# Optimization experiments

Hardware: AMD Instinct MI355X
Metric: run time of the kernel (lower is better)

Reference implementation:

```python
import jax, jax.numpy as jnp
import numpy as np

N_FEATURES = 1024
N_HEADS = 16
D_ATTN = 64


def setup_inputs() -> dict:
    key = jax.random.key(0)
    k_x, k_qkv, k_pw, k_pb = jax.random.split(key, 4)
    B, S = 2, 2048
    x = jax.random.normal(k_x, (B, S, N_FEATURES), dtype=jnp.float32)
    # torch nn.Linear weights are [out, in]; init scale ~ 1/sqrt(in)
    w_qkv = jax.random.normal(k_qkv, (3 * N_HEADS * D_ATTN, N_FEATURES), dtype=jnp.float32) / np.sqrt(N_FEATURES)
    w_proj = jax.random.normal(k_pw, (N_FEATURES, N_HEADS * D_ATTN), dtype=jnp.float32) / np.sqrt(N_HEADS * D_ATTN)
    b_proj = jax.random.normal(k_pb, (N_FEATURES,), dtype=jnp.float32) / np.sqrt(N_HEADS * D_ATTN)
    return {"x": x, "w_qkv": w_qkv, "w_proj": w_proj, "b_proj": b_proj}


def reference(x, w_qkv, w_proj, b_proj):
    B, S, F = x.shape
    H, D = N_HEADS, D_ATTN
    # fused QKV projection (bias=False): [B,S,3*H*D]
    qkv = jnp.einsum('bsf,of->bso', x, w_qkv)
    qkv = qkv.reshape(B, S, 3, H, D)
    q = jnp.transpose(qkv[:, :, 0], (0, 2, 1, 3))  # [B,H,S,D]
    k = jnp.transpose(qkv[:, :, 1], (0, 2, 1, 3))
    v = jnp.transpose(qkv[:, :, 2], (0, 2, 1, 3))
    scale = 1.0 / jnp.sqrt(jnp.asarray(D, dtype=x.dtype))
    scores = jnp.einsum('bhqd,bhkd->bhqk', q, k) * scale  # [B,H,S,S]
    attn = jax.nn.softmax(scores, axis=-1)
    out = jnp.einsum('bhqk,bhkd->bhqd', attn, v)  # [B,H,S,D]
    out = jnp.transpose(out, (0, 2, 1, 3)).reshape(B, S, H * D)
    # output projection (dropout is identity in eval mode)
    return jnp.einsum('bsm,fm->bsf', out, w_proj) + b_proj
```

## Files before the change

kernel.cpp:

```cpp
#include <hip/hip_runtime.h>
#include <hip/hip_bf16.h>
#include <math.h>

#define BATCH 2
#define SEQ 2048
#define NFEAT 1024
#define NHEAD 16
#define DHEAD 64
#define MROWS (BATCH * SEQ)
#define NQKV (3 * NHEAD * DHEAD)

typedef __attribute__((ext_vector_type(8))) short short8;
typedef __attribute__((ext_vector_type(4))) float floatx4;

#define CEXP 0.18033688f

__device__ __forceinline__ unsigned short f2bf(float f) {
    unsigned int u = __float_as_uint(f);
    u += 0x7fff + ((u >> 16) & 1);
    return (unsigned short)(u >> 16);
}

__device__ __forceinline__ float fast_exp2(float x) {
    return __builtin_amdgcn_exp2f(x);
}

__device__ __forceinline__ uint pack_bf16x2(float lo, float hi) {
    float2 t; t.x = lo; t.y = hi;
    __hip_bfloat162 h = __float22bfloat162_rn(t);
    union { __hip_bfloat162 h; uint u; } c; c.h = h;
    return c.u;
}

__device__ __forceinline__ void async16(const void* g, void* l) {
    __builtin_amdgcn_global_load_lds(
        (const __attribute__((address_space(1))) void*)g,
        (__attribute__((address_space(3))) void*)l, 16, 0, 0);
}

__global__ void cvt_swz(const float* __restrict__ x, const float* __restrict__ wq,
                        const float* __restrict__ wp,
                        ushort* __restrict__ xb, ushort* __restrict__ wqb,
                        ushort* __restrict__ wpb) {
    const int NX = MROWS * NFEAT / 4, NWQ = NQKV * NFEAT / 4, NWP = NFEAT * NFEAT / 4;
    int i = blockIdx.x * blockDim.x + threadIdx.x;
    if (i >= NX + NWQ + NWP) return;
    const float* src; ushort* dst; int idx4;
    if (i < NX)            { src = x;  dst = xb;  idx4 = i; }
    else if (i < NX + NWQ) { src = wq; dst = wqb; idx4 = i - NX; }
    else                   { src = wp; dst = wpb; idx4 = i - NX - NWQ; }
    float4 v = ((const float4*)src)[idx4];
    ushort4 o;
    o.x = f2bf(v.x); o.y = f2bf(v.y); o.z = f2bf(v.z); o.w = f2bf(v.w);
    const int e = idx4 * 4;
    const int k = e & (NFEAT - 1);
    const int row = e >> 10;
    const int kp = (k & ~31) | (((((k >> 3) & 3) ^ ((row >> 1) & 3))) << 3) | (k & 7);
    *(ushort4*)(dst + (size_t)row * NFEAT + kp) = o;
}

__global__ __launch_bounds__(256, 2)
void gemm_qkv(const ushort* __restrict__ A, const ushort* __restrict__ W,
              ushort* __restrict__ qb, ushort* __restrict__ kb, ushort* __restrict__ vtb) {
    __shared__ ushort smem[8192];
    ushort* As = smem;
    ushort* Bs = smem + 4096;
    const int tid = threadIdx.x;
    const int wave = tid >> 6, lane = tid & 63;
    const int m0 = blockIdx.y * 128, n0 = blockIdx.x * 128;
    const int wm = (wave >> 1) * 64, wn = (wave & 1) * 64;
    const int lr = lane & 15, lg = lane >> 4;
    const int kswz = (lg ^ ((lr >> 1) & 3)) * 8;

    floatx4 acc[4][4] = {};

    const int seg0 = tid, seg1 = tid + 256;
    const int row0 = seg0 >> 2, cb0 = (seg0 & 3) * 8;
    const int row1 = seg1 >> 2, cb1 = (seg1 & 3) * 8;

    for (int k0 = 0; k0 < NFEAT; k0 += 32) {
        async16(A + (size_t)(m0 + row0) * NFEAT + k0 + cb0, (void*)(As + seg0 * 8));
        async16(A + (size_t)(m0 + row1) * NFEAT + k0 + cb1, (void*)(As + seg1 * 8));
        async16(W + (size_t)(n0 + row0) * NFEAT + k0 + cb0, (void*)(Bs + seg0 * 8));
        async16(W + (size_t)(n0 + row1) * NFEAT + k0 + cb1, (void*)(Bs + seg1 * 8));
        __syncthreads();
        short8 a[4], b[4];
#pragma unroll
        for (int i = 0; i < 4; ++i)
            a[i] = *(const short8*)(As + (wm + i * 16 + lr) * 32 + kswz);
#pragma unroll
        for (int j = 0; j < 4; ++j)
            b[j] = *(const short8*)(Bs + (wn + j * 16 + lr) * 32 + kswz);
#pragma unroll
        for (int i = 0; i < 4; ++i)
#pragma unroll
            for (int j = 0; j < 4; ++j)
                acc[i][j] = __builtin_amdgcn_mfma_f32_16x16x32_bf16(a[i], b[j], acc[i][j], 0, 0, 0);
        __syncthreads();
    }

    const int t = n0 >> 10;
    const int bidx = m0 >> 11;
    if (t < 2) {
#pragma unroll
        for (int i = 0; i < 4; ++i)
#pragma unroll
            for (int j = 0; j < 4; ++j)
#pragma unroll
                for (int r = 0; r < 4; ++r) {
                    const int m = m0 + wm + i * 16 + lg * 4 + r;
                    const int n = n0 + wn + j * 16 + lr;
                    const int s = m & (SEQ - 1);
                    const int rem = n & 1023, h = rem >> 6, d = rem & 63;
                    if (t == 0) {
                        qb[((size_t)(bidx * NHEAD + h) * SEQ + s) * DHEAD + d] =
                            f2bf(acc[i][j][r] * CEXP);
                    } else {
                        const int dcol = ((((d >> 3) ^ (s & 7)) << 3)) | (d & 7);
                        kb[((size_t)(bidx * NHEAD + h) * SEQ + s) * DHEAD + dcol] =
                            f2bf(acc[i][j][r]);
                    }
                }
    } else {
#pragma unroll
        for (int hhalf = 0; hhalf < 2; ++hhalf) {
            if ((wm >> 6) == hhalf) {
#pragma unroll
                for (int i = 0; i < 4; ++i) {
                    const int chunk = i * 2 + (lg >> 1);
#pragma unroll
                    for (int j = 0; j < 4; ++j) {
                        const int n = wn + j * 16 + lr;
                        uint2 pk;
                        pk.x = pack_bf16x2(acc[i][j][0], acc[i][j][1]);
                        pk.y = pack_bf16x2(acc[i][j][2], acc[i][j][3]);
                        *(uint2*)(smem + n * 64 + ((chunk ^ (n & 7)) * 8) + (lg & 1) * 4) = pk;
                    }
                }
            }
            __syncthreads();
            const int s_base = (m0 & (SEQ - 1)) + hhalf * 64;
#pragma unroll
            for (int it = 0; it < 4; ++it) {
                const int n_r = (tid >> 3) + it * 32;
                const int p = tid & 7;
                short8 rowv = *(const short8*)(smem + n_r * 64 + p * 8);
                const int nglob = n0 + n_r;
                const int d = nglob & 63, hh = (nglob & 1023) >> 6;
                *(short8*)(vtb + ((size_t)(bidx * NHEAD + hh) * DHEAD + d) * SEQ + s_base + p * 8) = rowv;
            }
            __syncthreads();
        }
    }
}

__global__ __launch_bounds__(256, 2)
void gemm_proj(const ushort* __restrict__ A, const ushort* __restrict__ W,
               const float* __restrict__ bias, float* __restrict__ Cout) {
    __shared__ ushort As[128 * 32];
    __shared__ ushort Bs[64 * 32];
    const int tid = threadIdx.x;
    const int wave = tid >> 6, lane = tid & 63;
    const int m0 = blockIdx.y * 128, n0 = blockIdx.x * 64;
    const int wm = (wave >> 1) * 64, wn = (wave & 1) * 32;
    const int lr = lane & 15, lg = lane >> 4;
    const int kswz = (lg ^ ((lr >> 1) & 3)) * 8;

    floatx4 acc[4][2] = {};

    const int rowA = tid >> 2, cb = (tid & 3) * 8;

    for (int k0 = 0; k0 < NFEAT; k0 += 32) {
        async16(A + (size_t)(m0 + rowA) * NFEAT + k0 + cb, (void*)(As + tid * 8));
        async16(A + (size_t)(m0 + rowA + 64) * NFEAT + k0 + cb, (void*)(As + (tid + 256) * 8));
        async16(W + (size_t)(n0 + rowA) * NFEAT + k0 + cb, (void*)(Bs + tid * 8));
        __syncthreads();
        short8 a[4], b[2];
#pragma unroll
        for (int i = 0; i < 4; ++i)
            a[i] = *(const short8*)(As + (wm + i * 16 + lr) * 32 + kswz);
#pragma unroll
        for (int j = 0; j < 2; ++j)
            b[j] = *(const short8*)(Bs + (wn + j * 16 + lr) * 32 + kswz);
#pragma unroll
        for (int i = 0; i < 4; ++i)
#pragma unroll
            for (int j = 0; j < 2; ++j)
                acc[i][j] = __builtin_amdgcn_mfma_f32_16x16x32_bf16(a[i], b[j], acc[i][j], 0, 0, 0);
        __syncthreads();
    }

#pragma unroll
    for (int i = 0; i < 4; ++i)
#pragma unroll
        for (int j = 0; j < 2; ++j)
#pragma unroll
            for (int r = 0; r < 4; ++r) {
                const int m = m0 + wm + i * 16 + lg * 4 + r;
                const int n = n0 + wn + j * 16 + lr;
                Cout[(size_t)m * NFEAT + n] = acc[i][j][r] + bias[n];
            }
}

__global__ __launch_bounds__(256, 2)
void flash_attn(const ushort* __restrict__ qb, const ushort* __restrict__ kb,
                const ushort* __restrict__ vtb, ushort* __restrict__ aob) {
    const int qt = blockIdx.x, bh = blockIdx.y;
    const int tid = threadIdx.x, wave = tid >> 6, lane = tid & 63;
    const int lr = lane & 15, lg = lane >> 4;

    __shared__ ushort Ks[2][64 * 64];
    __shared__ ushort Vs[2][64 * 64];
    __shared__ ushort Ps_all[4][32 * 64];
    ushort* Ps = Ps_all[wave];

    const ushort* Qb = qb + (size_t)bh * SEQ * DHEAD;
    const ushort* Kb = kb + (size_t)bh * SEQ * DHEAD;
    const ushort* Vt = vtb + (size_t)bh * DHEAD * SEQ;

    const int q0 = qt * 128 + wave * 32;

    short8 qf[2][2];
#pragma unroll
    for (int j = 0; j < 2; ++j)
#pragma unroll
        for (int kk = 0; kk < 2; ++kk)
            qf[j][kk] = *(const short8*)(Qb + (size_t)(q0 + j * 16 + lr) * DHEAD + kk * 32 + lg * 8);

    const int kofs = tid * 8;
    const size_t vrow = (size_t)(tid >> 3) * SEQ;
    const int vcol = (tid & 7) * 8;

    async16(Kb + kofs,                    (void*)(Ks[0] + kofs));
    async16(Kb + 2048 + kofs,             (void*)(Ks[0] + 2048 + kofs));
    async16(Vt + vrow + vcol,             (void*)(Vs[0] + kofs));
    async16(Vt + 32 * SEQ + vrow + vcol,  (void*)(Vs[0] + 2048 + kofs));

    floatx4 acc_o[2][4] = {};
    float l_lane[2] = {0.0f, 0.0f};
    const int sw = lr & 7;

#define FLASH_PREFETCH(BUF, KV)                                                     \
    {                                                                               \
        const int kv_ = (KV);                                                       \
        async16(Kb + (size_t)kv_ * DHEAD + kofs,          (void*)(Ks[BUF] + kofs)); \
        async16(Kb + (size_t)kv_ * DHEAD + 2048 + kofs,   (void*)(Ks[BUF] + 2048 + kofs)); \
        async16(Vt + vrow + kv_ + vcol,                   (void*)(Vs[BUF] + kofs)); \
        async16(Vt + 32 * SEQ + vrow + kv_ + vcol,        (void*)(Vs[BUF] + 2048 + kofs)); \
    }

#define FLASH_COMPUTE(BUF)                                                          \
    {                                                                               \
        floatx4 st[4][2] = {};                                                      \
        _Pragma("unroll")                                                           \
        for (int kk = 0; kk < 2; ++kk)                                              \
            _Pragma("unroll")                                                       \
            for (int i = 0; i < 4; ++i) {                                           \
                short8 kf = *(const short8*)(Ks[BUF] + (i * 16 + lr) * 64 +         \
                                             (((kk * 4 + lg) ^ sw) * 8));           \
                _Pragma("unroll")                                                   \
                for (int j = 0; j < 2; ++j)                                         \
                    st[i][j] = __builtin_amdgcn_mfma_f32_16x16x32_bf16(kf, qf[j][kk], st[i][j], 0, 0, 0); \
            }                                                                       \
        _Pragma("unroll")                                                           \
        for (int i = 0; i < 4; ++i)                                                 \
            _Pragma("unroll")                                                       \
            for (int j = 0; j < 2; ++j) {                                           \
                const float p0 = fast_exp2(st[i][j][0]);                            \
                const float p1 = fast_exp2(st[i][j][1]);                            \
                const float p2 = fast_exp2(st[i][j][2]);                            \
                const float p3 = fast_exp2(st[i][j][3]);                            \
                l_lane[j] += (p0 + p1) + (p2 + p3);                                 \
                uint2 pk;                                                           \
                pk.x = pack_bf16x2(p0, p1);                                         \
                pk.y = pack_bf16x2(p2, p3);                                         \
                const int chunk = i * 2 + (lg >> 1);                                \
                *(uint2*)(Ps + (j * 16 + lr) * 64 + ((chunk ^ sw) * 8) + (lg & 1) * 4) = pk; \
            }                                                                       \
        _Pragma("unroll")                                                           \
        for (int kk2 = 0; kk2 < 2; ++kk2) {                                         \
            short8 vf[4];                                                           \
            _Pragma("unroll")                                                       \
            for (int j2 = 0; j2 < 4; ++j2)                                          \
                vf[j2] = *(const short8*)(Vs[BUF] + (j2 * 16 + lr) * 64 +           \
                                          (((kk2 * 4 + lg) ^ sw) * 8));             \
            _Pragma("unroll")                                                       \
            for (int i2 = 0; i2 < 2; ++i2) {                                        \
                short8 pf = *(const short8*)(Ps + (i2 * 16 + lr) * 64 +             \
                                             (((kk2 * 4 + lg) ^ sw) * 8));          \
                _Pragma("unroll")                                                   \
                for (int j2 = 0; j2 < 4; ++j2)                                      \
                    acc_o[i2][j2] = __builtin_amdgcn_mfma_f32_16x16x32_bf16(pf, vf[j2], acc_o[i2][j2], 0, 0, 0); \
            }                                                                       \
        }                                                                           \
    }

    for (int kt = 0; kt < SEQ / 64; kt += 2) {
        __syncthreads();
        FLASH_PREFETCH(1, (kt + 1) * 64)
        FLASH_COMPUTE(0)
        __syncthreads();
        if (kt + 2 < SEQ / 64)
            FLASH_PREFETCH(0, (kt + 2) * 64)
        FLASH_COMPUTE(1)
    }
#undef FLASH_PREFETCH
#undef FLASH_COMPUTE

#pragma unroll
    for (int j = 0; j < 2; ++j) {
        l_lane[j] += __shfl_xor(l_lane[j], 16);
        l_lane[j] += __shfl_xor(l_lane[j], 32);
    }

    const int b = bh >> 4, h = bh & 15;
#pragma unroll
    for (int i2 = 0; i2 < 2; ++i2) {
#pragma unroll
        for (int r = 0; r < 4; ++r) {
            const float lq = __shfl(l_lane[i2], lg * 4 + r);
            const float invl = 1.0f / lq;
            const int srow = b * SEQ + q0 + i2 * 16 + lg * 4 + r;
            const int key = (srow >> 1) & 3;
#pragma unroll
            for (int j2 = 0; j2 < 4; ++j2) {
                const int d = j2 * 16 + lr;
                const int dsw = (d & ~31) | (((((d >> 3) & 3) ^ key)) << 3) | (d & 7);
                aob[(size_t)srow * (NHEAD * DHEAD) + h * DHEAD + dsw] = f2bf(acc_o[i2][j2][r] * invl);
            }
        }
    }
}

extern "C" void kernel_launch(void* const* d_in, const int* in_sizes, int n_in,
                              void* d_out, int out_size, void* d_ws, size_t ws_size,
                              hipStream_t stream) {
    const float* x      = (const float*)d_in[0];
    const float* w_qkv  = (const float*)d_in[1];
    const float* w_proj = (const float*)d_in[2];
    const float* b_proj = (const float*)d_in[3];
    float* out = (float*)d_out;

    ushort* ws = (ushort*)d_ws;
    ushort* xb     = ws;
    ushort* wqkvb  = xb + (size_t)MROWS * NFEAT;
    ushort* wprojb = wqkvb + (size_t)NQKV * NFEAT;
    ushort* qb     = wprojb + (size_t)NFEAT * NFEAT;
    ushort* kb     = qb + (size_t)MROWS * NFEAT;
    ushort* vtb    = kb + (size_t)MROWS * NFEAT;
    ushort* aob    = vtb + (size_t)MROWS * NFEAT;

    {
        const int total = (MROWS * NFEAT + NQKV * NFEAT + NFEAT * NFEAT) / 4;
        cvt_swz<<<(total + 255) / 256, 256, 0, stream>>>(x, w_qkv, w_proj, xb, wqkvb, wprojb);
    }

    {
        dim3 grid(NQKV / 128, MROWS / 128);
        gemm_qkv<<<grid, 256, 0, stream>>>(xb, wqkvb, qb, kb, vtb);
    }

    {
        dim3 grid(SEQ / 128, BATCH * NHEAD);
        flash_attn<<<grid, 256, 0, stream>>>(qb, kb, vtb, aob);
    }

    {
        dim3 grid(NFEAT / 64, MROWS / 128);
        gemm_proj<<<grid, 256, 0, stream>>>(aob, wprojb, b_proj, out);
    }
}
```

Before: 187.9 us.

## Split attention KV range across two blocks and combine partial outputs

Flash attention now splits the key/value sequence into two halves along a new grid dimension. Each block writes unnormalized partial outputs and row sums to reused workspace buffers, and a new combine kernel adds the halves, normalizes them and writes the swizzled layout the projection GEMM expects. The change also shrinks the K tile to 32 rows, uses a padded P buffer stride, and raises launch-bounds occupancy hints. The aim is more blocks in flight and more occupancy on the attention stage, at the cost of an extra kernel and extra memory traffic. Partials are rounded to bf16 before being combined, which may cost some accuracy. No running max is subtracted, so the scores are apparently pre-scaled.

Measured after the change: 189.3 us. Within noise of the previous version (+0.7%).

```diff
diff --git a/kernel.cpp b/kernel.cpp
--- a/kernel.cpp
+++ b/kernel.cpp
@@ -19,6 +19,10 @@
     unsigned int u = __float_as_uint(f);
     u += 0x7fff + ((u >> 16) & 1);
     return (unsigned short)(u >> 16);
+}
+
+__device__ __forceinline__ float bf2f(unsigned short u) {
+    return __uint_as_float((unsigned int)u << 16);
 }
 
 __device__ __forceinline__ float fast_exp2(float x) {
@@ -59,7 +63,7 @@
     *(ushort4*)(dst + (size_t)row * NFEAT + kp) = o;
 }
 
-__global__ __launch_bounds__(256, 2)
+__global__ __launch_bounds__(256, 3)
 void gemm_qkv(const ushort* __restrict__ A, const ushort* __restrict__ W,
               ushort* __restrict__ qb, ushort* __restrict__ kb, ushort* __restrict__ vtb) {
     __shared__ ushort smem[8192];
@@ -202,16 +206,19 @@
             }
 }
 
-__global__ __launch_bounds__(256, 2)
+#define PSTRIDE 40
+__global__ __launch_bounds__(256, 4)
 void flash_attn(const ushort* __restrict__ qb, const ushort* __restrict__ kb,
-                const ushort* __restrict__ vtb, ushort* __restrict__ aob) {
-    const int qt = blockIdx.x, bh = blockIdx.y;
+                const ushort* __restrict__ vtb,
+                ushort* __restrict__ op0, ushort* __restrict__ op1,
+                float* __restrict__ lp0, float* __restrict__ lp1) {
+    const int qt = blockIdx.x, ks = blockIdx.y, bh = blockIdx.z;
     const int tid = threadIdx.x, wave = tid >> 6, lane = tid & 63;
     const int lr = lane & 15, lg = lane >> 4;
 
-    __shared__ ushort Ks[2][64 * 64];
+    __shared__ ushort Ks[2][32 * 64];
     __shared__ ushort Vs[2][64 * 64];
-    __shared__ ushort Ps_all[4][32 * 64];
+    __shared__ ushort Ps_all[4][32 * PSTRIDE];
     ushort* Ps = Ps_all[wave];
 
     const ushort* Qb = qb + (size_t)bh * SEQ * DHEAD;
@@ -219,6 +226,7 @@
     const ushort* Vt = vtb + (size_t)bh * DHEAD * SEQ;
 
     const int q0 = qt * 128 + wave * 32;
+    const int kvbase = ks * (SEQ / 2);
 
     short8 qf[2][2];
 #pragma unroll
@@ -227,43 +235,38 @@
         for (int kk = 0; kk < 2; ++kk)
             qf[j][kk] = *(const short8*)(Qb + (size_t)(q0 + j * 16 + lr) * DHEAD + kk * 32 + lg * 8);
 
-    const int kofs = tid * 8;
+    const int krow = tid >> 3, kseg = (tid & 7) * 8;
     const size_t vrow = (size_t)(tid >> 3) * SEQ;
-    const int vcol = (tid & 7) * 8;
-
-    async16(Kb + kofs,                    (void*)(Ks[0] + kofs));
-    async16(Kb + 2048 + kofs,             (void*)(Ks[0] + 2048 + kofs));
-    async16(Vt + vrow + vcol,             (void*)(Vs[0] + kofs));
-    async16(Vt + 32 * SEQ + vrow + vcol,  (void*)(Vs[0] + 2048 + kofs));
+    const int vseg = (tid & 7) * 8;
+
+#define STAGE_K(BUF, KV0) \
+    async16(Kb + (size_t)((KV0) + krow) * DHEAD + kseg, (void*)(Ks[BUF] + tid * 8));
+#define STAGE_V(BUF, KV0) \
+    async16(Vt + vrow + (KV0) + vseg,            (void*)(Vs[BUF] + tid * 8)); \
+    async16(Vt + 32 * SEQ + vrow + (KV0) + vseg, (void*)(Vs[BUF] + 2048 + tid * 8));
+
+    STAGE_K(0, kvbase)
+    STAGE_V(0, kvbase)
 
     floatx4 acc_o[2][4] = {};
     float l_lane[2] = {0.0f, 0.0f};
     const int sw = lr & 7;
 
-#define FLASH_PREFETCH(BUF, KV)                                                     \
+#define FLASH_COMPUTE(KBUF, VB, KVH)                                                \
     {                                                                               \
-        const int kv_ = (KV);                                                       \
-        async16(Kb + (size_t)kv_ * DHEAD + kofs,          (void*)(Ks[BUF] + kofs)); \
-        async16(Kb + (size_t)kv_ * DHEAD + 2048 + kofs,   (void*)(Ks[BUF] + 2048 + kofs)); \
-        async16(Vt + vrow + kv_ + vcol,                   (void*)(Vs[BUF] + kofs)); \
-        async16(Vt + 32 * SEQ + vrow + kv_ + vcol,        (void*)(Vs[BUF] + 2048 + kofs)); \
-    }
-
-#define FLASH_COMPUTE(BUF)                                                          \
-    {                                                                               \
-        floatx4 st[4][2] = {};                                                      \
+        floatx4 st[2][2] = {};                                                      \
         _Pragma("unroll")                                                           \
         for (int kk = 0; kk < 2; ++kk)                                              \
             _Pragma("unroll")                                                       \
-            for (int i = 0; i < 4; ++i) {                                           \
-                short8 kf = *(const short8*)(Ks[BUF] + (i * 16 + lr) * 64 +         \
+            for (int i = 0; i < 2; ++i) {                                           \
+                short8 kf = *(const short8*)(Ks[KBUF] + (i * 16 + lr) * 64 +        \
                                              (((kk * 4 + lg) ^ sw) * 8));           \
                 _Pragma("unroll")                                                   \
                 for (int j = 0; j < 2; ++j)                                         \
                     st[i][j] = __builtin_amdgcn_mfma_f32_16x16x32_bf16(kf, qf[j][kk], st[i][j], 0, 0, 0); \
             }                                                                       \
         _Pragma("unroll")                                                           \
-        for (int i = 0; i < 4; ++i)                                                 \
+        for (int i = 0; i < 2; ++i)                                                 \
             _Pragma("unroll")                                                       \
             for (int j = 0; j < 2; ++j) {                                           \
                 const float p0 = fast_exp2(st[i][j][0]);                            \
@@ -274,20 +277,17 @@
                 uint2 pk;                                                           \
                 pk.x = pack_bf16x2(p0, p1);                                         \
                 pk.y = pack_bf16x2(p2, p3);                                         \
-                const int chunk = i * 2 + (lg >> 1);                                \
-                *(uint2*)(Ps + (j * 16 + lr) * 64 + ((chunk ^ sw) * 8) + (lg & 1) * 4) = pk; \
+                *(uint2*)(Ps + (j * 16 + lr) * PSTRIDE + i * 16 + lg * 4) = pk;     \
             }                                                                       \
-        _Pragma("unroll")                                                           \
-        for (int kk2 = 0; kk2 < 2; ++kk2) {                                         \
+        {                                                                           \
             short8 vf[4];                                                           \
             _Pragma("unroll")                                                       \
             for (int j2 = 0; j2 < 4; ++j2)                                          \
-                vf[j2] = *(const short8*)(Vs[BUF] + (j2 * 16 + lr) * 64 +           \
-                                          (((kk2 * 4 + lg) ^ sw) * 8));             \
+                vf[j2] = *(const short8*)(Vs[VB] + (j2 * 16 + lr) * 64 +            \
+                                          ((((KVH) * 4 + lg) ^ sw) * 8));           \
             _Pragma("unroll")                                                       \
             for (int i2 = 0; i2 < 2; ++i2) {                                        \
-                short8 pf = *(const short8*)(Ps + (i2 * 16 + lr) * 64 +             \
-                                             (((kk2 * 4 + lg) ^ sw) * 8));          \
+                short8 pf = *(const short8*)(Ps + (i2 * 16 + lr) * PSTRIDE + lg * 8); \
                 _Pragma("unroll")                                                   \
                 for (int j2 = 0; j2 < 4; ++j2)                                      \
                     acc_o[i2][j2] = __builtin_amdgcn_mfma_f32_16x16x32_bf16(pf, vf[j2], acc_o[i2][j2], 0, 0, 0); \
@@ -295,41 +295,74 @@
         }                                                                           \
     }
 
-    for (int kt = 0; kt < SEQ / 64; kt += 2) {
-        __syncthreads();
-        FLASH_PREFETCH(1, (kt + 1) * 64)
-        FLASH_COMPUTE(0)
-        __syncthreads();
-        if (kt + 2 < SEQ / 64)
-            FLASH_PREFETCH(0, (kt + 2) * 64)
-        FLASH_COMPUTE(1)
-    }
-#undef FLASH_PREFETCH
+    const int NT = (SEQ / 2) / 32;
+    for (int t = 0; t < NT; t += 2) {
+        const int vb = (t >> 1) & 1;
+        __syncthreads();
+        STAGE_K(1, kvbase + (t + 1) * 32)
+        if (t + 2 < NT) { STAGE_V(1 - vb, kvbase + (t + 2) * 32) }
+        FLASH_COMPUTE(0, vb, 0)
+        __syncthreads();
+        if (t + 2 < NT) { STAGE_K(0, kvbase + (t + 2) * 32) }
+        FLASH_COMPUTE(1, vb, 1)
+    }
 #undef FLASH_COMPUTE
+#undef STAGE_K
+#undef STAGE_V
 
 #pragma unroll
     for (int j = 0; j < 2; ++j) {
         l_lane[j] += __shfl_xor(l_lane[j], 16);
         l_lane[j] += __shfl_xor(l_lane[j], 32);
     }
+    ushort* op = ks ? op1 : op0;
+    float* lp = ks ? lp1 : lp0;
+    if (lg == 0) {
+#pragma unroll
+        for (int j = 0; j < 2; ++j)
+            lp[(size_t)bh * SEQ + q0 + j * 16 + lr] = l_lane[j];
+    }
 
     const int b = bh >> 4, h = bh & 15;
 #pragma unroll
     for (int i2 = 0; i2 < 2; ++i2) {
 #pragma unroll
         for (int r = 0; r < 4; ++r) {
-            const float lq = __shfl(l_lane[i2], lg * 4 + r);
-            const float invl = 1.0f / lq;
             const int srow = b * SEQ + q0 + i2 * 16 + lg * 4 + r;
-            const int key = (srow >> 1) & 3;
 #pragma unroll
             for (int j2 = 0; j2 < 4; ++j2) {
                 const int d = j2 * 16 + lr;
-                const int dsw = (d & ~31) | (((((d >> 3) & 3) ^ key)) << 3) | (d & 7);
-                aob[(size_t)srow * (NHEAD * DHEAD) + h * DHEAD + dsw] = f2bf(acc_o[i2][j2][r] * invl);
+                op[(size_t)srow * (NHEAD * DHEAD) + h * DHEAD + d] = f2bf(acc_o[i2][j2][r]);
             }
         }
     }
+}
+
+__global__ void combine(const ushort* __restrict__ o0, const ushort* __restrict__ o1,
+                        const float* __restrict__ l0, const float* __restrict__ l1,
+                        ushort* __restrict__ aout) {
+    const int idx = blockIdx.x * 256 + threadIdx.x;
+    const int srow = idx >> 7;
+    const int k8 = (idx & 127) * 8;
+    const int b = srow >> 11, s = srow & (SEQ - 1);
+    const int h = k8 >> 6;
+    const size_t lidx = (size_t)(b * NHEAD + h) * SEQ + s;
+    const float inv = 1.0f / (l0[lidx] + l1[lidx]);
+    short8 a = *(const short8*)(o0 + (size_t)srow * NFEAT + k8);
+    short8 c = *(const short8*)(o1 + (size_t)srow * NFEAT + k8);
+    uint2 lohi[2];
+    uint pk[4];
+#pragma unroll
+    for (int e = 0; e < 4; ++e) {
+        const float f0 = (bf2f((unsigned short)a[2 * e]) + bf2f((unsigned short)c[2 * e])) * inv;
+        const float f1 = (bf2f((unsigned short)a[2 * e + 1]) + bf2f((unsigned short)c[2 * e + 1])) * inv;
+        pk[e] = pack_bf16x2(f0, f1);
+    }
+    lohi[0].x = pk[0]; lohi[0].y = pk[1]; lohi[1].x = pk[2]; lohi[1].y = pk[3];
+    const int cidx = (k8 >> 3) & 3, key = (srow >> 1) & 3;
+    const int kp = (k8 & ~31) | ((cidx ^ key) * 8);
+    *(uint2*)(aout + (size_t)srow * NFEAT + kp) = lohi[0];
+    *(uint2*)(aout + (size_t)srow * NFEAT + kp + 4) = lohi[1];
 }
 
 extern "C" void kernel_launch(void* const* d_in, const int* in_sizes, int n_in,
@@ -350,6 +383,12 @@
     ushort* vtb    = kb + (size_t)MROWS * NFEAT;
     ushort* aob    = vtb + (size_t)MROWS * NFEAT;
 
+    ushort* op0 = aob;
+    ushort* op1 = xb;
+    float* lp0 = (float*)wqkvb;
+    float* lp1 = lp0 + (size_t)BATCH * NHEAD * SEQ;
+    ushort* acmb = kb;
+
     {
         const int total = (MROWS * NFEAT + NQKV * NFEAT + NFEAT * NFEAT) / 4;
         cvt_swz<<<(total + 255) / 256, 256, 0, stream>>>(x, w_qkv, w_proj, xb, wqkvb, wprojb);
@@ -361,12 +400,17 @@
     }
 
     {
-        dim3 grid(SEQ / 128, BATCH * NHEAD);
-        flash_attn<<<grid, 256, 0, stream>>>(qb, kb, vtb, aob);
+        dim3 grid(SEQ / 128, 2, BATCH * NHEAD);
+        flash_attn<<<grid, 256, 0, stream>>>(qb, kb, vtb, op0, op1, lp0, lp1);
+    }
+
+    {
+        const int total = MROWS * (NFEAT / 8);
+        combine<<<total / 256, 256, 0, stream>>>(op0, op1, lp0, lp1, acmb);
     }
 
     {
         dim3 grid(NFEAT / 64, MROWS / 128);
-        gemm_proj<<<grid, 256, 0, stream>>>(aob, wprojb, b_proj, out);
-    }
-}
+        gemm_proj<<<grid, 256, 0, stream>>>(acmb, wprojb, b_proj, out);
+    }
+}
```
